# Kernel optimization log

Measured on AMD Instinct MI355X. Metric: run time of the kernel, lower is better.

The kernel has to match this reference:

```python
import jax, jax.numpy as jnp
import numpy as np

NUM_HEADS = 16
WINDOW = 128
PERSIST = 16


def setup_inputs() -> dict:
    key = jax.random.key(0)
    ks = jax.random.split(key, 6)
    B, S, D, L = 2, 2048, 2048, 512
    sd = 1.0 / np.sqrt(D)
    sl = 1.0 / np.sqrt(L)
    return {
        "x": jax.random.normal(ks[0], (B, S, D), dtype=jnp.float32),
        "Wq": jax.random.normal(ks[1], (D, D), dtype=jnp.float32) * sd,
        "Wkv": jax.random.normal(ks[2], (D, L), dtype=jnp.float32) * sd,
        "Wk": jax.random.normal(ks[3], (L, D), dtype=jnp.float32) * sl,
        "Wv": jax.random.normal(ks[4], (L, D), dtype=jnp.float32) * sl,
        "Wo": jax.random.normal(ks[5], (D, D), dtype=jnp.float32) * sd,
    }


def reference(x, Wq, Wkv, Wk, Wv, Wo):
    B, S, D = x.shape
    H = NUM_HEADS
    hd = D // H
    scale = hd ** -0.5

    q = (x @ Wq).reshape(B, S, H, hd)
    kv_latent = x @ Wkv                      # MLA-style latent bottleneck
    k = (kv_latent @ Wk).reshape(B, S, H, hd)
    v = (kv_latent @ Wv).reshape(B, S, H, hd)

    # causal + sliding-window + persistent attention-sink mask
    qi = jnp.arange(S)[:, None]
    ki = jnp.arange(S)[None, :]
    mask = (ki <= qi) & ((qi - ki < WINDOW) | (ki < PERSIST))  # [S,S]

    scores = jnp.einsum("bqhd,bkhd->bhqk", q, k) * scale
    scores = jnp.where(mask[None, None], scores, jnp.finfo(scores.dtype).min)
    attn = jax.nn.softmax(scores, axis=-1)
    out = jnp.einsum("bhqk,bkhd->bqhd", attn, v).reshape(B, S, D)
    return out @ Wo
```

## Files before the change

kernel.cpp:

```cpp
#include <hip/hip_runtime.h>

typedef float f32x4 __attribute__((ext_vector_type(4)));
typedef float f32x16 __attribute__((ext_vector_type(16)));
typedef __bf16 bf16x8 __attribute__((ext_vector_type(8)));
typedef short short8 __attribute__((ext_vector_type(8)));

__device__ __forceinline__ short f2bf(float f) {
    union { float f; unsigned u; } x; x.f = f;
    unsigned r = x.u + 0x7fffu + ((x.u >> 16) & 1u);
    return (short)(r >> 16);
}
__device__ __forceinline__ float bf2f(short s) {
    union { unsigned u; float f; } x;
    x.u = ((unsigned)(unsigned short)s) << 16;
    return x.f;
}

__device__ __forceinline__ void store_out(float* p, float v) { *p = v; }
__device__ __forceinline__ void store_out(short* p, float v) { *p = f2bf(v); }

__device__ __forceinline__ void gload_lds16(const short* g, short* l) {
    __builtin_amdgcn_global_load_lds(
        (__attribute__((address_space(1))) void*)(void*)g,
        (__attribute__((address_space(3))) void*)l, 16, 0, 0);
}

__global__ void prep_all(const float* __restrict__ x, short* __restrict__ xb,
                         const float* __restrict__ Wq, const float* __restrict__ Wo,
                         const float* __restrict__ Wk, const float* __restrict__ Wv,
                         const float* __restrict__ Wkv,
                         short* __restrict__ WqkvT, short* __restrict__ WoT,
                         short* __restrict__ WkT, short* __restrict__ WvT) {
    __shared__ float tile[32][33];
    int id = blockIdx.x;
    const int t = threadIdx.x;
    if (id < 8192) {
        const int i = id * 256 + t;
        float4 v = ((const float4*)x)[i];
        ((short4*)xb)[i] = make_short4(f2bf(v.x), f2bf(v.y), f2bf(v.z), f2bf(v.w));
        return;
    }
    id -= 8192;
    const float* in; short* out; int R, C, xt, yt;
    if (id < 4096)       { in = Wq;  out = WqkvT; R = 2048; C = 2048; xt = id & 63; yt = id >> 6; }
    else if (id < 8192)  { id -= 4096; in = Wo;  out = WoT;  R = 2048; C = 2048; xt = id & 63; yt = id >> 6; }
    else if (id < 9216)  { id -= 8192; in = Wk;  out = WkT;  R = 512;  C = 2048; xt = id & 63; yt = id >> 6; }
    else if (id < 10240) { id -= 9216; in = Wv;  out = WvT;  R = 512;  C = 2048; xt = id & 63; yt = id >> 6; }
    else                 { id -= 10240; in = Wkv; out = WqkvT + (size_t)2048 * 2048;
                           R = 2048; C = 512; xt = id & 15; yt = id >> 4; }
    const int c0 = xt * 32, r0 = yt * 32;
    const int tx = t & 31, ty = t >> 5;
#pragma unroll
    for (int i = 0; i < 32; i += 8)
        tile[ty + i][tx] = in[(size_t)(r0 + ty + i) * C + c0 + tx];
    __syncthreads();
#pragma unroll
    for (int i = 0; i < 32; i += 8)
        out[(size_t)(c0 + ty + i) * R + r0 + tx] = f2bf(tile[tx][ty + i]);
}

template <typename OutT>
__device__ __forceinline__ void gemm32_core(
    const short* __restrict__ A, const short* __restrict__ Bt, OutT* __restrict__ C,
    int m0, int n0, int K, int lda, int ldb, int ldc, short* sA, short* sB) {
    const int t = threadIdx.x;
    const int w = t >> 6, l = t & 63;
    const int wr = w >> 1, wc = w & 1;
    const int lrow = l & 31, lhalf = l >> 5;

    f32x16 acc[2][2] = {};

    const int r_off = w * 32 + (l >> 3);
    const int c8 = (((l & 7) ^ (l >> 3)) & 7) * 8;
    const short* aB = A + (size_t)(m0 + r_off) * lda + c8;
    const short* bB = Bt + (size_t)(n0 + r_off) * ldb + c8;
    short* sAw = sA + w * 2048;
    short* sBw = sB + w * 2048;

    for (int kk = 0; kk < K; kk += 64) {
#pragma unroll
        for (int p = 0; p < 4; ++p) {
            gload_lds16(aB + kk + (size_t)(p * 8) * lda, sAw + p * 512);
            gload_lds16(bB + kk + (size_t)(p * 8) * ldb, sBw + p * 512);
        }
        __syncthreads();
#pragma unroll
        for (int ks = 0; ks < 4; ++ks) {
            const int c = ks * 2 + lhalf;
            bf16x8 af[2], bfr[2];
#pragma unroll
            for (int mi = 0; mi < 2; ++mi) {
                const int m = wr * 64 + mi * 32 + lrow;
                af[mi] = *(const bf16x8*)&sA[m * 64 + (c ^ (m & 7)) * 8];
            }
#pragma unroll
            for (int ni = 0; ni < 2; ++ni) {
                const int n = wc * 64 + ni * 32 + lrow;
                bfr[ni] = *(const bf16x8*)&sB[n * 64 + (c ^ (n & 7)) * 8];
            }
#pragma unroll
            for (int mi = 0; mi < 2; ++mi)
#pragma unroll
                for (int ni = 0; ni < 2; ++ni)
                    acc[mi][ni] = __builtin_amdgcn_mfma_f32_32x32x16_bf16(
                        af[mi], bfr[ni], acc[mi][ni], 0, 0, 0);
        }
        __syncthreads();
    }
#pragma unroll
    for (int mi = 0; mi < 2; ++mi)
#pragma unroll
        for (int ni = 0; ni < 2; ++ni) {
            const int col = n0 + wc * 64 + ni * 32 + lrow;
#pragma unroll
            for (int r = 0; r < 16; ++r) {
                const int row = m0 + wr * 64 + mi * 32 + (r & 3) + 8 * (r >> 2) + 4 * lhalf;
                store_out(&C[(size_t)row * ldc + col], acc[mi][ni][r]);
            }
        }
}

template <typename OutT>
__global__ __launch_bounds__(256, 2)
void gemm32(const short* __restrict__ A, const short* __restrict__ Bt,
            OutT* __restrict__ C, int K, int lda, int ldb, int ldc) {
    __shared__ __align__(16) short sA[128 * 64];
    __shared__ __align__(16) short sB[128 * 64];
    gemm32_core<OutT>(A, Bt, C, blockIdx.y * 128, blockIdx.x * 128, K, lda, ldb, ldc, sA, sB);
}

__global__ __launch_bounds__(256, 2)
void gemm32_kv(const short* __restrict__ kvl, const short* __restrict__ WkT,
               short* __restrict__ kk, const short* __restrict__ WvT,
               short* __restrict__ vT) {
    __shared__ __align__(16) short sA[128 * 64];
    __shared__ __align__(16) short sB[128 * 64];
    int id = blockIdx.x;
    if (id < 512) {
        gemm32_core<short>(kvl, WkT, kk, (id >> 4) * 128, (id & 15) * 128,
                           512, 2560, 512, 2048, sA, sB);
    } else {
        id -= 512;
        gemm32_core<short>(WvT, kvl, vT, (id >> 5) * 128, (id & 31) * 128,
                           512, 512, 2560, 4096, sA, sB);
    }
}

#define A_S 2048
#define A_D 2048
#define A_M 4096
#define A_HD 128
__global__ __launch_bounds__(256)
void attn_win3(const short* __restrict__ Q, const short* __restrict__ K,
               const short* __restrict__ vT, short* __restrict__ O, int ldq) {
    const int qt = blockIdx.x, h = blockIdx.y, b = blockIdx.z;
    const int Qs = qt * 64;
    const int t = threadIdx.x, w = t >> 6, l = t & 63;
    const int qs = Qs + w * 16;
    const int lg = l >> 4, ln = l & 15;
    const float SCALE = 0.088388347648318447f;

    __shared__ __align__(16) short sK[2][512 * 8];
    __shared__ __align__(16) short sV[2][512 * 8];
    __shared__ __align__(16) short sP[4][16][40];

    const size_t bS = (size_t)b * A_S;
    const short* qrow = Q + (bS + qs + ln) * ldq + h * A_HD;
    bf16x8 qf[4];
#pragma unroll
    for (int ks = 0; ks < 4; ++ks)
        qf[ks] = *(const bf16x8*)(qrow + ks * 32 + lg * 8);

    f32x4 o[8] = {};
    float lsum[4] = {0.f, 0.f, 0.f, 0.f};

    int C_lo = (Qs - 127) >> 5; if (C_lo < 0) C_lo = 0;
    const int C_hi = (Qs + 63) >> 5;
    const bool sink = C_lo > 0;
    const int total = (C_hi - C_lo + 1) + (sink ? 1 : 0);

    const int key0 = t >> 4, dseg0s = (t & 15) ^ (key0 & 7);
    const int d0 = t >> 2, ksg0 = (t & 3) ^ ((d0 >> 1) & 3);
    const int key1 = (256 + t) >> 4, dseg1s = (t & 15) ^ (key1 & 7);
    const int d1 = (256 + t) >> 2, ksg1 = (t & 3) ^ ((d1 >> 1) & 3);
    const short* Kb = K + bS * A_D + h * A_HD;
    const short* Vb = vT + (size_t)h * A_HD * A_M + b * A_S;

#define STAGE(kb, buf)                                                          \
    do {                                                                        \
        gload_lds16(Kb + (size_t)((kb) + key0) * A_D + dseg0s * 8,              \
                    &sK[buf][(size_t)(w * 64) * 8]);                            \
        gload_lds16(Vb + (size_t)d0 * A_M + (kb) + ksg0 * 8,                    \
                    &sV[buf][(size_t)(w * 64) * 8]);                            \
        gload_lds16(Kb + (size_t)((kb) + key1) * A_D + dseg1s * 8,              \
                    &sK[buf][(size_t)(256 + w * 64) * 8]);                      \
        gload_lds16(Vb + (size_t)d1 * A_M + (kb) + ksg1 * 8,                    \
                    &sV[buf][(size_t)(256 + w * 64) * 8]);                      \
    } while (0)

#define CHUNK_KB(ci) ((((sink) && (ci) == 0) ? 0 : (C_lo + (ci) - (sink ? 1 : 0))) * 32)

    STAGE(CHUNK_KB(0), 0);
    __syncthreads();

    for (int ci = 0; ci < total; ++ci) {
        if (ci + 1 < total) {
            const int nkb = CHUNK_KB(ci + 1);
            STAGE(nkb, (ci + 1) & 1);
        }
        const int kb = CHUNK_KB(ci);
        const int buf = ci & 1;
        const bool any = (kb < 16) || ((kb + 31 >= qs - 127) && (kb <= qs + 15));
        if (any) {
            f32x4 s0 = {0.f, 0.f, 0.f, 0.f}, s1 = {0.f, 0.f, 0.f, 0.f};
#pragma unroll
            for (int ks = 0; ks < 4; ++ks) {
                const int dsg = ks * 4 + lg;
                bf16x8 k0 = *(const bf16x8*)&sK[buf][(ln * 16 + (dsg ^ (ln & 7))) * 8];
                bf16x8 k1 = *(const bf16x8*)&sK[buf][((16 + ln) * 16 + (dsg ^ (ln & 7))) * 8];
                s0 = __builtin_amdgcn_mfma_f32_16x16x32_bf16(qf[ks], k0, s0, 0, 0, 0);
                s1 = __builtin_amdgcn_mfma_f32_16x16x32_bf16(qf[ks], k1, s1, 0, 0, 0);
            }
            const int k0i = kb + ln, k1i = kb + 16 + ln;
#pragma unroll
            for (int r = 0; r < 4; ++r) {
                const int qi = qs + lg * 4 + r;
                const bool m0 = (k0i <= qi) && ((qi - k0i < 128) || (k0i < 16));
                const bool m1 = (k1i <= qi) && ((qi - k1i < 128) || (k1i < 16));
                const float p0 = m0 ? __expf(s0[r] * SCALE) : 0.f;
                const float p1 = m1 ? __expf(s1[r] * SCALE) : 0.f;
                lsum[r] += p0 + p1;
                sP[w][lg * 4 + r][ln] = f2bf(p0);
                sP[w][lg * 4 + r][16 + ln] = f2bf(p1);
            }
            bf16x8 pf = *(const bf16x8*)&sP[w][ln][lg * 8];
#pragma unroll
            for (int dgi = 0; dgi < 8; ++dgi) {
                const int d = dgi * 16 + ln;
                bf16x8 vf = *(const bf16x8*)&sV[buf][(d * 4 + (lg ^ ((ln >> 1) & 3))) * 8];
                o[dgi] = __builtin_amdgcn_mfma_f32_16x16x32_bf16(pf, vf, o[dgi], 0, 0, 0);
            }
        }
        __syncthreads();
    }
#undef STAGE
#undef CHUNK_KB

#pragma unroll
    for (int r = 0; r < 4; ++r) {
        float s = lsum[r];
        s += __shfl_xor(s, 1); s += __shfl_xor(s, 2);
        s += __shfl_xor(s, 4); s += __shfl_xor(s, 8);
        const float inv = 1.0f / s;
        short* orow = O + (bS + qs + lg * 4 + r) * A_D + h * A_HD + ln;
#pragma unroll
        for (int dgi = 0; dgi < 8; ++dgi)
            orow[dgi * 16] = f2bf(o[dgi][r] * inv);
    }
}

extern "C" void kernel_launch(void* const* d_in, const int* in_sizes, int n_in,
                              void* d_out, int out_size, void* d_ws, size_t ws_size,
                              hipStream_t stream) {
    (void)in_sizes; (void)n_in; (void)out_size; (void)ws_size;
    const float* x   = (const float*)d_in[0];
    const float* Wq  = (const float*)d_in[1];
    const float* Wkv = (const float*)d_in[2];
    const float* Wk  = (const float*)d_in[3];
    const float* Wv  = (const float*)d_in[4];
    const float* Wo  = (const float*)d_in[5];
    float* out = (float*)d_out;

    const int B = 2, S = 2048, D = 2048, L = 512, H = 16;
    const int M = B * S;
    const int NQ = D + L;

    short* p = (short*)d_ws;
    short* xb    = p; p += (size_t)M * D;
    short* WqkvT = p; p += (size_t)NQ * D;
    short* WkT   = p; p += (size_t)D * L;
    short* WvT   = p; p += (size_t)D * L;
    short* WoT   = p; p += (size_t)D * D;
    short* qkv   = p; p += (size_t)M * NQ;
    short* kk    = p; p += (size_t)M * D;
    short* vT    = p; p += (size_t)D * M;
    short* ao    = p; p += (size_t)M * D;

    prep_all<<<19456, 256, 0, stream>>>(x, xb, Wq, Wo, Wk, Wv, Wkv,
                                        WqkvT, WoT, WkT, WvT);
    gemm32<short><<<dim3(NQ / 128, M / 128), 256, 0, stream>>>(
        xb, WqkvT, qkv, D, D, D, NQ);
    gemm32_kv<<<1024, 256, 0, stream>>>(qkv + D, WkT, kk, WvT, vT);

    attn_win3<<<dim3(S / 64, H, B), 256, 0, stream>>>(qkv, kk, vT, ao, NQ);

    gemm32<float><<<dim3(D / 128, M / 128), 256, 0, stream>>>(
        ao, WoT, out, D, D, D, D);
}
```

Before: 279.0 us.

## Replace 128x128 GEMMs with 256x256 tiles and multi-stage LDS pipeline

Replaces the 128x128-tile, 4-wave GEMM with a 256x256-tile, 8-wave kernel that uses 128KB of dynamic LDS split into double-buffered half-K stages. Global-to-LDS loads are issued ahead and tracked with explicit vmcnt waits, raw s_barrier calls and setprio around the MFMA bursts, and 16x16x32 MFMAs replace 32x32. The aim is more data reuse per tile and overlap of loads with compute. The cost is fewer blocks per GEMM (for example 160 for the QKV projection on a 256-CU part), which risks under-filling the device, plus a fragile hand-written synchronisation scheme.

```diff
diff --git a/kernel.cpp b/kernel.cpp
--- a/kernel.cpp
+++ b/kernel.cpp
@@ -1,19 +1,12 @@
 #include <hip/hip_runtime.h>
 
 typedef float f32x4 __attribute__((ext_vector_type(4)));
-typedef float f32x16 __attribute__((ext_vector_type(16)));
 typedef __bf16 bf16x8 __attribute__((ext_vector_type(8)));
-typedef short short8 __attribute__((ext_vector_type(8)));
 
 __device__ __forceinline__ short f2bf(float f) {
     union { float f; unsigned u; } x; x.f = f;
     unsigned r = x.u + 0x7fffu + ((x.u >> 16) & 1u);
     return (short)(r >> 16);
-}
-__device__ __forceinline__ float bf2f(short s) {
-    union { unsigned u; float f; } x;
-    x.u = ((unsigned)(unsigned short)s) << 16;
-    return x.f;
 }
 
 __device__ __forceinline__ void store_out(float* p, float v) { *p = v; }
@@ -59,90 +52,147 @@
         out[(size_t)(c0 + ty + i) * R + r0 + tx] = f2bf(tile[tx][ty + i]);
 }
 
+#define LBASE(buf, kh, ab) ((((((buf) << 1) | (kh)) << 1) | (ab)) * 8192)
+
+#define STAGE(P, ld, tt, kh, buf, ab)                                   \
+    do {                                                                \
+        const int kb_ = (tt) * 64 + (kh) * 32;                          \
+        const short* s_ = (P) + kb_;                                    \
+        short* d_ = lds + LBASE(buf, kh, ab) + w * 512;                 \
+        gload_lds16(s_, d_);                                            \
+        gload_lds16(s_ + (size_t)128 * (ld), d_ + 4096);                \
+    } while (0)
+
+#define VM6 asm volatile("s_waitcnt vmcnt(6)" ::: "memory")
+
+#define MFMA16(a, b, c) __builtin_amdgcn_mfma_f32_16x16x32_bf16(a, b, c, 0, 0, 0)
+
+#define MM_ROW(mi, areg)                                                \
+    acc[mi][0] = MFMA16(areg, bv0, acc[mi][0]);                         \
+    acc[mi][1] = MFMA16(areg, bv1, acc[mi][1]);                         \
+    acc[mi][2] = MFMA16(areg, bv2, acc[mi][2]);                         \
+    acc[mi][3] = MFMA16(areg, bv3, acc[mi][3]);
+
+#define HALFK(buf, kh, STG0, W0, STG1)                                  \
+    {                                                                   \
+        bf16x8 bv0, bv1, bv2, bv3;                                      \
+        {                                                               \
+            const short* Ab_ = lds + LBASE(buf, kh, 0) + (wm * 128) * 32 + foff; \
+            const short* Bb_ = lds + LBASE(buf, kh, 1) + (wn * 64) * 32 + foff;  \
+            bf16x8 a0_ = *(const bf16x8*)&Ab_[0];                       \
+            bf16x8 a1_ = *(const bf16x8*)&Ab_[512];                     \
+            bf16x8 a2_ = *(const bf16x8*)&Ab_[1024];                    \
+            bf16x8 a3_ = *(const bf16x8*)&Ab_[1536];                    \
+            bv0 = *(const bf16x8*)&Bb_[0];                              \
+            bv1 = *(const bf16x8*)&Bb_[512];                            \
+            bv2 = *(const bf16x8*)&Bb_[1024];                           \
+            bv3 = *(const bf16x8*)&Bb_[1536];                           \
+            STG0;                                                       \
+            W0;                                                         \
+            __builtin_amdgcn_s_barrier();                               \
+            asm volatile("s_waitcnt lgkmcnt(0)" ::: "memory");          \
+            __builtin_amdgcn_sched_barrier(0);                          \
+            __builtin_amdgcn_s_setprio(1);                              \
+            MM_ROW(0, a0_) MM_ROW(1, a1_) MM_ROW(2, a2_) MM_ROW(3, a3_) \
+            __builtin_amdgcn_s_setprio(0);                              \
+            __builtin_amdgcn_s_barrier();                               \
+        }                                                               \
+        {                                                               \
+            const short* Ab_ = lds + LBASE(buf, kh, 0) + (wm * 128 + 64) * 32 + foff; \
+            bf16x8 a0_ = *(const bf16x8*)&Ab_[0];                       \
+            bf16x8 a1_ = *(const bf16x8*)&Ab_[512];                     \
+            bf16x8 a2_ = *(const bf16x8*)&Ab_[1024];                    \
+            bf16x8 a3_ = *(const bf16x8*)&Ab_[1536];                    \
+            STG1;                                                       \
+            __builtin_amdgcn_s_barrier();                               \
+            asm volatile("s_waitcnt lgkmcnt(0)" ::: "memory");          \
+            __builtin_amdgcn_sched_barrier(0);                          \
+            __builtin_amdgcn_s_setprio(1);                              \
+            MM_ROW(4, a0_) MM_ROW(5, a1_) MM_ROW(6, a2_) MM_ROW(7, a3_) \
+            __builtin_amdgcn_s_setprio(0);                              \
+            __builtin_amdgcn_s_barrier();                               \
+        }                                                               \
+    }
+
 template <typename OutT>
-__device__ __forceinline__ void gemm32_core(
+__device__ __forceinline__ void gemm256_core(
     const short* __restrict__ A, const short* __restrict__ Bt, OutT* __restrict__ C,
-    int m0, int n0, int K, int lda, int ldb, int ldc, short* sA, short* sB) {
+    int m0, int n0, int K, int lda, int ldb, int ldc, short* lds) {
     const int t = threadIdx.x;
     const int w = t >> 6, l = t & 63;
-    const int wr = w >> 1, wc = w & 1;
-    const int lrow = l & 31, lhalf = l >> 5;
-
-    f32x16 acc[2][2] = {};
-
-    const int r_off = w * 32 + (l >> 3);
-    const int c8 = (((l & 7) ^ (l >> 3)) & 7) * 8;
-    const short* aB = A + (size_t)(m0 + r_off) * lda + c8;
-    const short* bB = Bt + (size_t)(n0 + r_off) * ldb + c8;
-    short* sAw = sA + w * 2048;
-    short* sBw = sB + w * 2048;
-
-    for (int kk = 0; kk < K; kk += 64) {
-#pragma unroll
-        for (int p = 0; p < 4; ++p) {
-            gload_lds16(aB + kk + (size_t)(p * 8) * lda, sAw + p * 512);
-            gload_lds16(bB + kk + (size_t)(p * 8) * ldb, sBw + p * 512);
+    const int wm = w >> 2, wn = w & 3;
+    const int l15 = l & 15, lc = l >> 4;
+
+    const int srow = (w << 4) + (l >> 2);
+    const int scc8 = (((l & 3) ^ (((l >> 2) + (l >> 4)) & 3)) << 3);
+    const short* Ag = A + (size_t)(m0 + srow) * lda + scc8;
+    const short* Bg = Bt + (size_t)(n0 + srow) * ldb + scc8;
+
+    const int gl = (l15 + (l15 >> 2)) & 3;
+    const int foff = (l15 * 4 + (lc ^ gl)) * 8;
+
+    f32x4 acc[8][4] = {};
+
+    const int ntm1 = (K >> 6) - 1;
+    const int niter = K >> 7;
+
+    STAGE(Ag, lda, 0, 0, 0, 0);
+    STAGE(Bg, ldb, 0, 0, 0, 1);
+    STAGE(Ag, lda, 0, 1, 0, 0);
+    STAGE(Bg, ldb, 0, 1, 0, 1);
+    STAGE(Ag, lda, 1, 0, 1, 0);
+    STAGE(Bg, ldb, 1, 0, 1, 1);
+    asm volatile("s_waitcnt vmcnt(8)" ::: "memory");
+    __builtin_amdgcn_s_barrier();
+
+#pragma unroll 1
+    for (int it = 0; it < niter; ++it) {
+        const int tt = it * 2;
+        const int t1 = tt + 1;
+        const int t2 = (tt + 2 > ntm1) ? ntm1 : tt + 2;
+        const int t3 = (tt + 3 > ntm1) ? ntm1 : tt + 3;
+        HALFK(0, 0, STAGE(Ag, lda, t1, 1, 1, 0), VM6, STAGE(Bg, ldb, t1, 1, 1, 1))
+        HALFK(0, 1, STAGE(Ag, lda, t2, 0, 0, 0), VM6, STAGE(Bg, ldb, t2, 0, 0, 1))
+        HALFK(1, 0, STAGE(Ag, lda, t2, 1, 0, 0), VM6, STAGE(Bg, ldb, t2, 1, 0, 1))
+        HALFK(1, 1, STAGE(Ag, lda, t3, 0, 1, 0), VM6, STAGE(Bg, ldb, t3, 0, 1, 1))
+    }
+
+    asm volatile("s_waitcnt vmcnt(0)" ::: "memory");
+
+    const int crow = m0 + wm * 128 + lc * 4;
+    const int ccol = n0 + wn * 64 + l15;
+#pragma unroll
+    for (int mi = 0; mi < 8; ++mi)
+#pragma unroll
+        for (int ni = 0; ni < 4; ++ni) {
+            OutT* cp = C + (size_t)(crow + mi * 16) * ldc + ccol + ni * 16;
+#pragma unroll
+            for (int rr = 0; rr < 4; ++rr)
+                store_out(cp + (size_t)rr * ldc, acc[mi][ni][rr]);
         }
-        __syncthreads();
-#pragma unroll
-        for (int ks = 0; ks < 4; ++ks) {
-            const int c = ks * 2 + lhalf;
-            bf16x8 af[2], bfr[2];
-#pragma unroll
-            for (int mi = 0; mi < 2; ++mi) {
-                const int m = wr * 64 + mi * 32 + lrow;
-                af[mi] = *(const bf16x8*)&sA[m * 64 + (c ^ (m & 7)) * 8];
-            }
-#pragma unroll
-            for (int ni = 0; ni < 2; ++ni) {
-                const int n = wc * 64 + ni * 32 + lrow;
-                bfr[ni] = *(const bf16x8*)&sB[n * 64 + (c ^ (n & 7)) * 8];
-            }
-#pragma unroll
-            for (int mi = 0; mi < 2; ++mi)
-#pragma unroll
-                for (int ni = 0; ni < 2; ++ni)
-                    acc[mi][ni] = __builtin_amdgcn_mfma_f32_32x32x16_bf16(
-                        af[mi], bfr[ni], acc[mi][ni], 0, 0, 0);
-        }
-        __syncthreads();
-    }
-#pragma unroll
-    for (int mi = 0; mi < 2; ++mi)
-#pragma unroll
-        for (int ni = 0; ni < 2; ++ni) {
-            const int col = n0 + wc * 64 + ni * 32 + lrow;
-#pragma unroll
-            for (int r = 0; r < 16; ++r) {
-                const int row = m0 + wr * 64 + mi * 32 + (r & 3) + 8 * (r >> 2) + 4 * lhalf;
-                store_out(&C[(size_t)row * ldc + col], acc[mi][ni][r]);
-            }
-        }
 }
 
 template <typename OutT>
-__global__ __launch_bounds__(256, 2)
-void gemm32(const short* __restrict__ A, const short* __restrict__ Bt,
-            OutT* __restrict__ C, int K, int lda, int ldb, int ldc) {
-    __shared__ __align__(16) short sA[128 * 64];
-    __shared__ __align__(16) short sB[128 * 64];
-    gemm32_core<OutT>(A, Bt, C, blockIdx.y * 128, blockIdx.x * 128, K, lda, ldb, ldc, sA, sB);
-}
-
-__global__ __launch_bounds__(256, 2)
-void gemm32_kv(const short* __restrict__ kvl, const short* __restrict__ WkT,
-               short* __restrict__ kk, const short* __restrict__ WvT,
-               short* __restrict__ vT) {
-    __shared__ __align__(16) short sA[128 * 64];
-    __shared__ __align__(16) short sB[128 * 64];
+__global__ __launch_bounds__(512, 2)
+void gemm256(const short* __restrict__ A, const short* __restrict__ Bt,
+             OutT* __restrict__ C, int K, int lda, int ldb, int ldc) {
+    extern __shared__ short lds[];
+    gemm256_core<OutT>(A, Bt, C, blockIdx.y * 256, blockIdx.x * 256, K, lda, ldb, ldc, lds);
+}
+
+__global__ __launch_bounds__(512, 2)
+void gemm256_kv(const short* __restrict__ kvl, const short* __restrict__ WkT,
+                short* __restrict__ kk, const short* __restrict__ WvT,
+                short* __restrict__ vT) {
+    extern __shared__ short lds[];
     int id = blockIdx.x;
-    if (id < 512) {
-        gemm32_core<short>(kvl, WkT, kk, (id >> 4) * 128, (id & 15) * 128,
-                           512, 2560, 512, 2048, sA, sB);
+    if (id < 128) {
+        gemm256_core<short>(kvl, WkT, kk, (id >> 3) * 256, (id & 7) * 256,
+                            512, 2560, 512, 2048, lds);
     } else {
-        id -= 512;
-        gemm32_core<short>(WvT, kvl, vT, (id >> 5) * 128, (id & 31) * 128,
-                           512, 512, 2560, 4096, sA, sB);
+        id -= 128;
+        gemm256_core<short>(WvT, kvl, vT, (id >> 4) * 256, (id & 15) * 256,
+                            512, 512, 2560, 4096, lds);
     }
 }
 
@@ -186,7 +236,7 @@
     const short* Kb = K + bS * A_D + h * A_HD;
     const short* Vb = vT + (size_t)h * A_HD * A_M + b * A_S;
 
-#define STAGE(kb, buf)                                                          \
+#define ASTAGE(kb, buf)                                                         \
     do {                                                                        \
         gload_lds16(Kb + (size_t)((kb) + key0) * A_D + dseg0s * 8,              \
                     &sK[buf][(size_t)(w * 64) * 8]);                            \
@@ -200,13 +250,13 @@
 
 #define CHUNK_KB(ci) ((((sink) && (ci) == 0) ? 0 : (C_lo + (ci) - (sink ? 1 : 0))) * 32)
 
-    STAGE(CHUNK_KB(0), 0);
+    ASTAGE(CHUNK_KB(0), 0);
     __syncthreads();
 
     for (int ci = 0; ci < total; ++ci) {
         if (ci + 1 < total) {
             const int nkb = CHUNK_KB(ci + 1);
-            STAGE(nkb, (ci + 1) & 1);
+            ASTAGE(nkb, (ci + 1) & 1);
         }
         const int kb = CHUNK_KB(ci);
         const int buf = ci & 1;
@@ -243,7 +293,7 @@
         }
         __syncthreads();
     }
-#undef STAGE
+#undef ASTAGE
 #undef CHUNK_KB
 
 #pragma unroll
@@ -286,14 +336,25 @@
     short* vT    = p; p += (size_t)D * M;
     short* ao    = p; p += (size_t)M * D;
 
+    static bool attr_done = false;
+    if (!attr_done) {
+        hipFuncSetAttribute((const void*)&gemm256<short>,
+                            hipFuncAttributeMaxDynamicSharedMemorySize, 131072);
+        hipFuncSetAttribute((const void*)&gemm256<float>,
+                            hipFuncAttributeMaxDynamicSharedMemorySize, 131072);
+        hipFuncSetAttribute((const void*)&gemm256_kv,
+                            hipFuncAttributeMaxDynamicSharedMemorySize, 131072);
+        attr_done = true;
+    }
+
     prep_all<<<19456, 256, 0, stream>>>(x, xb, Wq, Wo, Wk, Wv, Wkv,
                                         WqkvT, WoT, WkT, WvT);
-    gemm32<short><<<dim3(NQ / 128, M / 128), 256, 0, stream>>>(
+    gemm256<short><<<dim3(NQ / 256, M / 256), 512, 131072, stream>>>(
         xb, WqkvT, qkv, D, D, D, NQ);
-    gemm32_kv<<<1024, 256, 0, stream>>>(qkv + D, WkT, kk, WvT, vT);
+    gemm256_kv<<<256, 512, 131072, stream>>>(qkv + D, WkT, kk, WvT, vT);
 
     attn_win3<<<dim3(S / 64, H, B), 256, 0, stream>>>(qkv, kk, vT, ao, NQ);
 
-    gemm32<float><<<dim3(D / 128, M / 128), 256, 0, stream>>>(
+    gemm256<float><<<dim3(D / 256, M / 256), 512, 131072, stream>>>(
         ao, WoT, out, D, D, D, D);
 }
```

New measurement: 292.8 us. 1.05x slower.
